# Kernel tuning notes

Hardware: AMD Instinct MI355X
Metric: run time of the kernel (lower is better)

Reference implementation:

```python
import jax, jax.numpy as jnp
import numpy as np

N_HEADS = 16


def setup_inputs() -> dict:
    key = jax.random.key(0)
    ks = jax.random.split(key, 9)
    B, S, D = 2, 2048, 1024
    s = 0.02
    return {
        "x": jax.random.normal(ks[0], (B, S, D), dtype=jnp.float32),
        "Wq": jax.random.normal(ks[1], (D, D), dtype=jnp.float32) * s,
        "bq": jax.random.normal(ks[2], (D,), dtype=jnp.float32) * s,
        "Wk": jax.random.normal(ks[3], (D, D), dtype=jnp.float32) * s,
        "bk": jax.random.normal(ks[4], (D,), dtype=jnp.float32) * s,
        "Wv": jax.random.normal(ks[5], (D, D), dtype=jnp.float32) * s,
        "bv": jax.random.normal(ks[6], (D,), dtype=jnp.float32) * s,
        "Wo": jax.random.normal(ks[7], (D, D), dtype=jnp.float32) * s,
        "bo": jax.random.normal(ks[8], (D,), dtype=jnp.float32) * s,
    }


def reference(x, Wq, bq, Wk, bk, Wv, bv, Wo, bo):
    B, S, D = x.shape
    H = N_HEADS
    hd = D // H
    # projections -> [B, H, S, hd]
    def heads(w, b):
        return (x @ w + b).reshape(B, S, H, hd).transpose(0, 2, 1, 3)
    Q, K, V = heads(Wq, bq), heads(Wk, bk), heads(Wv, bv)
    scores = jnp.einsum("bhqd,bhkd->bhqk", Q, K)
    causal = jnp.triu(jnp.ones((S, S), dtype=bool), k=1)  # True above diagonal
    scores = jnp.where(causal, -jnp.inf, scores)
    w = jax.nn.softmax(scores / jnp.sqrt(jnp.float32(hd)), axis=-1)
    ctx = jnp.einsum("bhqk,bhkd->bhqd", w, V).transpose(0, 2, 1, 3).reshape(B, S, D)
    return ctx @ Wo + bo
```

## Files before the change

### kernel.cpp

```cpp
#include <hip/hip_runtime.h>
#include <hip/hip_bf16.h>

typedef __attribute__((ext_vector_type(8))) short short8;
typedef __attribute__((ext_vector_type(4))) float floatx4;

#define D_MODEL 1024
#define SEQ     2048
#define NB      2
#define NH      16
#define HD      64
#define MROWS   4096
#define CZ      (0.125f * 1.44269504f)

__device__ __forceinline__ floatx4 mfma_bf16(short8 a, short8 b, floatx4 c) {
  return __builtin_amdgcn_mfma_f32_16x16x32_bf16(a, b, c, 0, 0, 0);
}

__device__ __forceinline__ void dma16(const __hip_bfloat16* g, __hip_bfloat16* l) {
  __builtin_amdgcn_global_load_lds(
      (const __attribute__((address_space(1))) void*)g,
      (__attribute__((address_space(3))) void*)l, 16, 0, 0);
}
#define WAIT_VM(n)  __asm__ __volatile__("s_waitcnt vmcnt(" #n ")" ::: "memory")
#define BARRIER()   __asm__ __volatile__("s_barrier" ::: "memory")
#define WAIT_LGKM() __asm__ __volatile__("s_waitcnt lgkmcnt(0)" ::: "memory")

__global__ void convert_x_kernel(const float* __restrict__ x, __hip_bfloat16* __restrict__ xb) {
  int i = (blockIdx.x * 256 + threadIdx.x) * 4;
  float4 v = *(const float4*)(x + i);
  __hip_bfloat16 tmp[4];
  tmp[0] = __float2bfloat16(v.x);
  tmp[1] = __float2bfloat16(v.y);
  tmp[2] = __float2bfloat16(v.z);
  tmp[3] = __float2bfloat16(v.w);
  *(ushort4*)(xb + i) = *(ushort4*)tmp;
}

__global__ void transpose_w_kernel(const float* __restrict__ W0, const float* __restrict__ W1,
                                   const float* __restrict__ W2, const float* __restrict__ W3,
                                   __hip_bfloat16* __restrict__ T0, __hip_bfloat16* __restrict__ T1,
                                   __hip_bfloat16* __restrict__ T2, __hip_bfloat16* __restrict__ T3) {
  const int z = blockIdx.z;
  const float* W = (z == 0) ? W0 : (z == 1) ? W1 : (z == 2) ? W2 : W3;
  __hip_bfloat16* Wt = (z == 0) ? T0 : (z == 1) ? T1 : (z == 2) ? T2 : T3;
  __shared__ float tile[32][33];
  int k0 = blockIdx.x * 32, n0 = blockIdx.y * 32;
  int tx = threadIdx.x, ty = threadIdx.y;
#pragma unroll
  for (int i = 0; i < 4; i++)
    tile[ty + 8 * i][tx] = W[(size_t)(k0 + ty + 8 * i) * D_MODEL + n0 + tx];
  __syncthreads();
#pragma unroll
  for (int i = 0; i < 4; i++)
    Wt[(size_t)(n0 + ty + 8 * i) * D_MODEL + k0 + tx] = __float2bfloat16(tile[tx][ty + 8 * i]);
}

template <int MODE>
__global__ __launch_bounds__(256) void gemm_kernel(
    const __hip_bfloat16* __restrict__ X,
    const __hip_bfloat16* __restrict__ Wt0, const __hip_bfloat16* __restrict__ Wt1,
    const __hip_bfloat16* __restrict__ Wt2,
    const float* __restrict__ b0, const float* __restrict__ b1, const float* __restrict__ b2,
    void* __restrict__ out0, void* __restrict__ out1, void* __restrict__ out2) {
  constexpr int MT = (MODE == 0) ? 128 : 64;
  constexpr int I = MT / 32;
  constexpr int NKT = D_MODEL / 32;

  const int z = blockIdx.y;
  const __hip_bfloat16* Wt = (z == 0) ? Wt0 : (z == 1) ? Wt1 : Wt2;
  const float* bias = (z == 0) ? b0 : (z == 1) ? b1 : b2;
  void* outp = (z == 0) ? out0 : (z == 1) ? out1 : out2;
  const float scale = (MODE == 0 && z == 0) ? CZ : 1.f;

  __shared__ __attribute__((aligned(16))) __hip_bfloat16 As[3][MT * 32];
  __shared__ __attribute__((aligned(16))) __hip_bfloat16 Bs[3][128 * 32];

  const int n0 = blockIdx.x * 128;
  const int m0 = blockIdx.z * MT;
  const int t = threadIdx.x;
  const int lane = t & 63, w = t >> 6;
  const int wm = (w >> 1) * (MT / 2), wn = (w & 1) * 64;
  const int lr = lane & 15;
  const int lq = lane >> 4;

  const __hip_bfloat16* Xp = X + (size_t)m0 * D_MODEL;
  const __hip_bfloat16* Wp = Wt + (size_t)n0 * D_MODEL;

  const int lrow = lane >> 2;
  const int skg = (lane & 3) << 3;
  const int srowA = ((MT == 128) ? (w << 5) : (w << 4)) + lrow;
  const int sbA0 = (((MT == 128) ? (w << 5) : (w << 4)) << 5);
  const int sbA1 = sbA0 + (16 << 5);
  const int srowB = (w << 5) + lrow;
  const int sbB0 = ((w << 5) << 5);
  const int sbB1 = sbB0 + (16 << 5);

#define STAGE_G(kt_, buf_)                                                              \
  {                                                                                     \
    const int kn_ = (kt_) * 32;                                                         \
    dma16(Xp + (size_t)srowA * D_MODEL + kn_ + skg, &As[buf_][sbA0]);                   \
    if (MT == 128) dma16(Xp + (size_t)(srowA + 16) * D_MODEL + kn_ + skg, &As[buf_][sbA1]); \
    dma16(Wp + (size_t)srowB * D_MODEL + kn_ + skg, &Bs[buf_][sbB0]);                   \
    dma16(Wp + (size_t)(srowB + 16) * D_MODEL + kn_ + skg, &Bs[buf_][sbB1]);            \
  }

  floatx4 acc[I][4];
#pragma unroll
  for (int i = 0; i < I; i++)
#pragma unroll
    for (int j = 0; j < 4; j++) acc[i][j] = (floatx4){0.f, 0.f, 0.f, 0.f};

  STAGE_G(0, 0);
  STAGE_G(1, 1);

  int cb = 0;
  for (int kt = 0; kt < NKT; kt++) {
    if (kt < NKT - 1) {
      if constexpr (MODE == 0) WAIT_VM(4);
      else                     WAIT_VM(3);
    } else {
      WAIT_VM(0);
    }
    BARRIER();
    if (kt + 2 < NKT) {
      const int nb = (cb == 0) ? 2 : cb - 1;
      STAGE_G(kt + 2, nb);
    }
    const __hip_bfloat16* Ac = As[cb];
    const __hip_bfloat16* Bc = Bs[cb];
    short8 af[I], bfr[4];
#pragma unroll
    for (int i = 0; i < I; i++) af[i] = *(const short8*)&Ac[(wm + i * 16 + lr) * 32 + lq * 8];
#pragma unroll
    for (int j = 0; j < 4; j++) bfr[j] = *(const short8*)&Bc[(wn + j * 16 + lr) * 32 + lq * 8];
#pragma unroll
    for (int i = 0; i < I; i++)
#pragma unroll
      for (int j = 0; j < 4; j++) acc[i][j] = mfma_bf16(af[i], bfr[j], acc[i][j]);
    cb = (cb == 2) ? 0 : cb + 1;
  }
#undef STAGE_G

#pragma unroll
  for (int j = 0; j < 4; j++) {
    const int n = n0 + wn + j * 16 + lr;
    const float bv = bias[n];
#pragma unroll
    for (int i = 0; i < I; i++) {
      const int mb = m0 + wm + i * 16 + lq * 4;
      if (MODE == 0) {
        __hip_bfloat16* O = (__hip_bfloat16*)outp;
        const int b = mb >> 11, s = mb & 2047;
        const int h = n >> 6, d = n & 63;
        if (z == 2) {
          ushort4 pk;
          __hip_bfloat16* pp = (__hip_bfloat16*)&pk;
#pragma unroll
          for (int r = 0; r < 4; r++) pp[r] = __float2bfloat16(acc[i][j][r] + bv);
          *(ushort4*)(O + (((size_t)(b * NH + h) * HD + d) * SEQ + s)) = pk;
        } else {
#pragma unroll
          for (int r = 0; r < 4; r++)
            O[(((size_t)(b * NH + h) * SEQ + (s + r)) * HD) + d] =
                __float2bfloat16((acc[i][j][r] + bv) * scale);
        }
      } else {
#pragma unroll
        for (int r = 0; r < 4; r++)
          ((float*)outp)[(size_t)(mb + r) * D_MODEL + n] = acc[i][j][r] + bv;
      }
    }
  }
}

__global__ __launch_bounds__(256, 2) void attn_kernel(
    const __hip_bfloat16* __restrict__ Q, const __hip_bfloat16* __restrict__ Kg,
    const __hip_bfloat16* __restrict__ Vt, __hip_bfloat16* __restrict__ ctx) {
  const int bh = blockIdx.x;
  const int b = bh >> 4, h = bh & 15;
  const int p = blockIdx.y;
  const int t = threadIdx.x, lane = t & 63, w = t >> 6;
  const int lr = lane & 15, lq = lane >> 4;

  __shared__ __attribute__((aligned(16))) __hip_bfloat16 Ks[3][64 * 64];
  __shared__ __attribute__((aligned(16))) __hip_bfloat16 VTs[3][64 * 64];
  __shared__ __attribute__((aligned(16))) __hip_bfloat16 Ps[4][16 * 72];

  const __hip_bfloat16* Qb = Q + (size_t)bh * SEQ * HD;
  const __hip_bfloat16* Kb = Kg + (size_t)bh * SEQ * HD;
  const __hip_bfloat16* Vb = Vt + (size_t)bh * HD * SEQ;

  short8 qf[2][2];
#pragma unroll
  for (int ph = 0; ph < 2; ph++) {
    const int qt = ph ? 31 - p : p;
    const int rw = qt * 64 + w * 16;
#pragma unroll
    for (int ks = 0; ks < 2; ks++)
      qf[ph][ks] = *(const short8*)(Qb + (size_t)(rw + lr) * HD + ks * 32 + lq * 8);
  }

  const int srow0 = (w << 4) + (lane >> 3);
  const int sgl = lane & 7;
  const int sb0 = ((w << 4) << 6);
  const int sb1 = (((w << 4) + 8) << 6);

  const int nkt0 = p + 1;
  const int TOT = 33;

#define STAGE(nn, nb)                                                                  \
  {                                                                                    \
    const int r0 = srow0, r1 = srow0 + 8;                                              \
    dma16(Kb + ((size_t)((nn) + r0) << 6) + ((sgl ^ (r0 & 7)) << 3), &Ks[nb][sb0]);    \
    dma16(Kb + ((size_t)((nn) + r1) << 6) + ((sgl ^ (r1 & 7)) << 3), &Ks[nb][sb1]);    \
    dma16(Vb + (size_t)r0 * SEQ + (nn) + ((sgl ^ (r0 & 7)) << 3), &VTs[nb][sb0]);      \
    dma16(Vb + (size_t)r1 * SEQ + (nn) + ((sgl ^ (r1 & 7)) << 3), &VTs[nb][sb1]);      \
  }
#define KTN(gs) (((gs) < nkt0) ? (gs) : (gs)-nkt0)

  STAGE(KTN(0) * 64, 0);
  STAGE(KTN(1) * 64, 1);
  int g = 0, cb = 0;

  for (int ph = 0; ph < 2; ph++) {
    const int qt = ph ? 31 - p : p;
    const int nkt = qt + 1;
    const int rw = qt * 64 + w * 16;

    floatx4 o[4];
#pragma unroll
    for (int dt = 0; dt < 4; dt++) o[dt] = (floatx4){0.f, 0.f, 0.f, 0.f};
    float ls[4] = {0.f, 0.f, 0.f, 0.f};

    for (int kt = 0; kt < nkt; kt++, g++) {
      if (g < TOT - 1) WAIT_VM(4);
      else             WAIT_VM(0);
      BARRIER();
      if (g + 2 < TOT) {
        const int nb = (cb == 0) ? 2 : cb - 1;
        STAGE(KTN(g + 2) * 64, nb);
      }
      const __hip_bfloat16* Kc = Ks[cb];
      const __hip_bfloat16* Vc = VTs[cb];
      cb = (cb == 2) ? 0 : cb + 1;
      __hip_bfloat16* PsW = Ps[w];

      floatx4 s[4];
#pragma unroll
      for (int nt = 0; nt < 4; nt++) s[nt] = (floatx4){0.f, 0.f, 0.f, 0.f};
#pragma unroll
      for (int ks = 0; ks < 2; ks++) {
#pragma unroll
        for (int nt = 0; nt < 4; nt++) {
          const int key = nt * 16 + lr;
          short8 kf = *(const short8*)&Kc[(key << 6) + (((ks * 4 + lq) ^ (key & 7)) << 3)];
          s[nt] = mfma_bf16(qf[ph][ks], kf, s[nt]);
        }
      }

      const int n0 = kt * 64;
      if (kt == nkt - 1) {
#pragma unroll
        for (int nt = 0; nt < 4; nt++)
#pragma unroll
          for (int r = 0; r < 4; r++) {
            const int row = rw + lq * 4 + r;
            const int key = n0 + nt * 16 + lr;
            float pe = (key <= row) ? exp2f(s[nt][r]) : 0.f;
            ls[r] += pe;
            PsW[(lq * 4 + r) * 72 + nt * 16 + lr] = __float2bfloat16(pe);
          }
      } else {
#pragma unroll
        for (int nt = 0; nt < 4; nt++)
#pragma unroll
          for (int r = 0; r < 4; r++) {
            float pe = exp2f(s[nt][r]);
            ls[r] += pe;
            PsW[(lq * 4 + r) * 72 + nt * 16 + lr] = __float2bfloat16(pe);
          }
      }
      WAIT_LGKM();

#pragma unroll
      for (int ks = 0; ks < 2; ks++) {
        short8 pf = *(const short8*)&PsW[lr * 72 + ks * 32 + lq * 8];
#pragma unroll
        for (int dt = 0; dt < 4; dt++) {
          const int d = dt * 16 + lr;
          short8 vf = *(const short8*)&Vc[(d << 6) + (((ks * 4 + lq) ^ (d & 7)) << 3)];
          o[dt] = mfma_bf16(pf, vf, o[dt]);
        }
      }
    }

    float inv[4];
#pragma unroll
    for (int r = 0; r < 4; r++) {
      float v = ls[r];
#pragma unroll
      for (int m = 8; m >= 1; m >>= 1) v += __shfl_xor(v, m, 16);
      inv[r] = 1.f / v;
    }
    __hip_bfloat16* cp = ctx + (size_t)b * SEQ * D_MODEL + h * HD;
#pragma unroll
    for (int dt = 0; dt < 4; dt++)
#pragma unroll
      for (int r = 0; r < 4; r++) {
        const int s = rw + lq * 4 + r;
        cp[(size_t)s * D_MODEL + dt * 16 + lr] = __float2bfloat16(o[dt][r] * inv[r]);
      }
  }
#undef STAGE
#undef KTN
}

extern "C" void kernel_launch(void* const* d_in, const int* in_sizes, int n_in,
                              void* d_out, int out_size, void* d_ws, size_t ws_size,
                              hipStream_t stream) {
  const float* x  = (const float*)d_in[0];
  const float* Wq = (const float*)d_in[1];
  const float* bq = (const float*)d_in[2];
  const float* Wk = (const float*)d_in[3];
  const float* bk = (const float*)d_in[4];
  const float* Wv = (const float*)d_in[5];
  const float* bv = (const float*)d_in[6];
  const float* Wo = (const float*)d_in[7];
  const float* bo = (const float*)d_in[8];

  char* ws = (char*)d_ws;
  const size_t MB = 1u << 20;
  __hip_bfloat16* xb  = (__hip_bfloat16*)(ws + 0 * MB);
  __hip_bfloat16* wtq = (__hip_bfloat16*)(ws + 8 * MB);
  __hip_bfloat16* wtk = (__hip_bfloat16*)(ws + 10 * MB);
  __hip_bfloat16* wtv = (__hip_bfloat16*)(ws + 12 * MB);
  __hip_bfloat16* wto = (__hip_bfloat16*)(ws + 14 * MB);
  __hip_bfloat16* qb  = (__hip_bfloat16*)(ws + 16 * MB);
  __hip_bfloat16* kb  = (__hip_bfloat16*)(ws + 24 * MB);
  __hip_bfloat16* vt  = (__hip_bfloat16*)(ws + 32 * MB);
  __hip_bfloat16* ctx = xb;

  convert_x_kernel<<<4096, 256, 0, stream>>>(x, xb);
  transpose_w_kernel<<<dim3(32, 32, 4), dim3(32, 8), 0, stream>>>(Wq, Wk, Wv, Wo,
                                                                  wtq, wtk, wtv, wto);
  gemm_kernel<0><<<dim3(8, 3, 32), 256, 0, stream>>>(xb, wtq, wtk, wtv, bq, bk, bv,
                                                     (void*)qb, (void*)kb, (void*)vt);
  attn_kernel<<<dim3(32, 16), 256, 0, stream>>>(qb, kb, vt, ctx);
  gemm_kernel<1><<<dim3(8, 1, 64), 256, 0, stream>>>(ctx, wto, wto, wto, bo, bo, bo,
                                                     d_out, d_out, d_out);
}
```

Baseline: 198.4 us.

## Split attention key tiles across two wave groups and keep P in registers

The attention block grows to 512 threads. Each pair of wave groups handles the two 64-key halves of a 128-key tile, and their partial outputs and row sums are merged through LDS at the end. The score MFMA is transposed so the exponentiated P can be reshuffled into operand layout with ds_bpermute instead of a round trip through shared memory. The triple-buffered 64-key staging becomes double-buffered 128-key staging with a full vmcnt wait every iteration. This adds memory-level parallelism but risks less load/compute overlap and idle diagonal waves.

```diff
diff --git a/kernel.cpp b/kernel.cpp
--- a/kernel.cpp
+++ b/kernel.cpp
@@ -3,6 +3,7 @@
 
 typedef __attribute__((ext_vector_type(8))) short short8;
 typedef __attribute__((ext_vector_type(4))) float floatx4;
+typedef __attribute__((ext_vector_type(4))) int intx4;
 
 #define D_MODEL 1024
 #define SEQ     2048
@@ -23,7 +24,12 @@
 }
 #define WAIT_VM(n)  __asm__ __volatile__("s_waitcnt vmcnt(" #n ")" ::: "memory")
 #define BARRIER()   __asm__ __volatile__("s_barrier" ::: "memory")
-#define WAIT_LGKM() __asm__ __volatile__("s_waitcnt lgkmcnt(0)" ::: "memory")
+
+__device__ __forceinline__ int packbf(float a, float b) {
+  union { __hip_bfloat16 h; unsigned short u; } x, y;
+  x.h = __float2bfloat16(a); y.h = __float2bfloat16(b);
+  return (int)(((unsigned)y.u << 16) | (unsigned)x.u);
+}
 
 __global__ void convert_x_kernel(const float* __restrict__ x, __hip_bfloat16* __restrict__ xb) {
   int i = (blockIdx.x * 256 + threadIdx.x) * 4;
@@ -173,7 +179,7 @@
   }
 }
 
-__global__ __launch_bounds__(256, 2) void attn_kernel(
+__global__ __launch_bounds__(512, 4) void attn_kernel(
     const __hip_bfloat16* __restrict__ Q, const __hip_bfloat16* __restrict__ Kg,
     const __hip_bfloat16* __restrict__ Vt, __hip_bfloat16* __restrict__ ctx) {
   const int bh = blockIdx.x;
@@ -181,10 +187,10 @@
   const int p = blockIdx.y;
   const int t = threadIdx.x, lane = t & 63, w = t >> 6;
   const int lr = lane & 15, lq = lane >> 4;
-
-  __shared__ __attribute__((aligned(16))) __hip_bfloat16 Ks[3][64 * 64];
-  __shared__ __attribute__((aligned(16))) __hip_bfloat16 VTs[3][64 * 64];
-  __shared__ __attribute__((aligned(16))) __hip_bfloat16 Ps[4][16 * 72];
+  const int wr = w & 3, wb = w >> 2;
+
+  __shared__ __attribute__((aligned(16))) __hip_bfloat16 Ks[2][128 * 64];
+  __shared__ __attribute__((aligned(16))) __hip_bfloat16 VTs[2][64 * 128];
 
   const __hip_bfloat16* Qb = Q + (size_t)bh * SEQ * HD;
   const __hip_bfloat16* Kb = Kg + (size_t)bh * SEQ * HD;
@@ -194,125 +200,168 @@
 #pragma unroll
   for (int ph = 0; ph < 2; ph++) {
     const int qt = ph ? 31 - p : p;
-    const int rw = qt * 64 + w * 16;
+    const int rw = qt * 64 + wr * 16;
 #pragma unroll
     for (int ks = 0; ks < 2; ks++)
       qf[ph][ks] = *(const short8*)(Qb + (size_t)(rw + lr) * HD + ks * 32 + lq * 8);
   }
 
-  const int srow0 = (w << 4) + (lane >> 3);
-  const int sgl = lane & 7;
-  const int sb0 = ((w << 4) << 6);
-  const int sb1 = (((w << 4) + 8) << 6);
-
-  const int nkt0 = p + 1;
-  const int TOT = 33;
-
-#define STAGE(nn, nb)                                                                  \
-  {                                                                                    \
-    const int r0 = srow0, r1 = srow0 + 8;                                              \
-    dma16(Kb + ((size_t)((nn) + r0) << 6) + ((sgl ^ (r0 & 7)) << 3), &Ks[nb][sb0]);    \
-    dma16(Kb + ((size_t)((nn) + r1) << 6) + ((sgl ^ (r1 & 7)) << 3), &Ks[nb][sb1]);    \
-    dma16(Vb + (size_t)r0 * SEQ + (nn) + ((sgl ^ (r0 & 7)) << 3), &VTs[nb][sb0]);      \
-    dma16(Vb + (size_t)r1 * SEQ + (nn) + ((sgl ^ (r1 & 7)) << 3), &VTs[nb][sb1]);      \
-  }
-#define KTN(gs) (((gs) < nkt0) ? (gs) : (gs)-nkt0)
-
-  STAGE(KTN(0) * 64, 0);
-  STAGE(KTN(1) * 64, 1);
-  int g = 0, cb = 0;
+  const int kr0 = (w << 4) + (lane >> 3);
+  const int kg0 = (lane & 7) ^ (kr0 & 7);
+  const int kr1 = kr0 + 8;
+  const int kg1 = (lane & 7) ^ (kr1 & 7);
+  const int kb0 = (w << 4) << 6;
+  const int kb1 = ((w << 4) + 8) << 6;
+  const int vr0 = (w << 3) + (lane >> 4);
+  const int vg0 = (lane & 15) ^ (vr0 & 15);
+  const int vr1 = vr0 + 4;
+  const int vg1 = (lane & 15) ^ (vr1 & 15);
+  const int vb0 = (w << 3) << 7;
+  const int vb1 = ((w << 3) + 4) << 7;
+
+  const int nktA = (p + 2) >> 1;
+  const int TOT = 17;
+
+#define STAGE(nn, nb)                                                           \
+  {                                                                             \
+    dma16(Kb + ((size_t)((nn) + kr0) << 6) + (kg0 << 3), &Ks[nb][kb0]);         \
+    dma16(Kb + ((size_t)((nn) + kr1) << 6) + (kg1 << 3), &Ks[nb][kb1]);         \
+    dma16(Vb + (size_t)vr0 * SEQ + (nn) + (vg0 << 3), &VTs[nb][vb0]);           \
+    dma16(Vb + (size_t)vr1 * SEQ + (nn) + (vg1 << 3), &VTs[nb][vb1]);           \
+  }
+
+  STAGE(0, 0);
+  int g = 0;
+
+  const int idx0 = (lr + ((lq & 1) << 5)) << 2;
+  const int idx1 = idx0 + 64;
+  const bool hi = (lq >= 2);
 
   for (int ph = 0; ph < 2; ph++) {
     const int qt = ph ? 31 - p : p;
-    const int nkt = qt + 1;
-    const int rw = qt * 64 + w * 16;
+    const int nkt = (qt + 2) >> 1;
+    const int rw = qt * 64 + wr * 16;
+    const int q = rw + lr;
 
     floatx4 o[4];
 #pragma unroll
     for (int dt = 0; dt < 4; dt++) o[dt] = (floatx4){0.f, 0.f, 0.f, 0.f};
-    float ls[4] = {0.f, 0.f, 0.f, 0.f};
+    float ls = 0.f;
 
     for (int kt = 0; kt < nkt; kt++, g++) {
-      if (g < TOT - 1) WAIT_VM(4);
-      else             WAIT_VM(0);
+      WAIT_VM(0);
       BARRIER();
-      if (g + 2 < TOT) {
-        const int nb = (cb == 0) ? 2 : cb - 1;
-        STAGE(KTN(g + 2) * 64, nb);
+      if (g + 1 < TOT) {
+        const int gn = g + 1;
+        const int ktn = (gn < nktA) ? gn : gn - nktA;
+        STAGE(ktn << 7, gn & 1);
       }
-      const __hip_bfloat16* Kc = Ks[cb];
-      const __hip_bfloat16* Vc = VTs[cb];
-      cb = (cb == 2) ? 0 : cb + 1;
-      __hip_bfloat16* PsW = Ps[w];
-
-      floatx4 s[4];
-#pragma unroll
-      for (int nt = 0; nt < 4; nt++) s[nt] = (floatx4){0.f, 0.f, 0.f, 0.f};
-#pragma unroll
-      for (int ks = 0; ks < 2; ks++) {
-#pragma unroll
-        for (int nt = 0; nt < 4; nt++) {
-          const int key = nt * 16 + lr;
-          short8 kf = *(const short8*)&Kc[(key << 6) + (((ks * 4 + lq) ^ (key & 7)) << 3)];
-          s[nt] = mfma_bf16(qf[ph][ks], kf, s[nt]);
+      const int n0 = (kt << 7) + (wb << 6);
+      if (n0 <= rw + 15) {
+        const __hip_bfloat16* Kc = Ks[g & 1];
+        const __hip_bfloat16* Vc = VTs[g & 1];
+
+        floatx4 s[4];
+#pragma unroll
+        for (int nt = 0; nt < 4; nt++) s[nt] = (floatx4){0.f, 0.f, 0.f, 0.f};
+#pragma unroll
+        for (int ks = 0; ks < 2; ks++) {
+#pragma unroll
+          for (int nt = 0; nt < 4; nt++) {
+            const int row = (wb << 6) + (nt << 4) + lr;
+            short8 kf = *(const short8*)&Kc[(row << 6) + ((((ks << 2) + lq) ^ (row & 7)) << 3)];
+            s[nt] = mfma_bf16(kf, qf[ph][ks], s[nt]);
+          }
         }
-      }
-
-      const int n0 = kt * 64;
-      if (kt == nkt - 1) {
-#pragma unroll
-        for (int nt = 0; nt < 4; nt++)
-#pragma unroll
-          for (int r = 0; r < 4; r++) {
-            const int row = rw + lq * 4 + r;
-            const int key = n0 + nt * 16 + lr;
-            float pe = (key <= row) ? exp2f(s[nt][r]) : 0.f;
-            ls[r] += pe;
-            PsW[(lq * 4 + r) * 72 + nt * 16 + lr] = __float2bfloat16(pe);
+
+        int pkA[4], pkB[4];
+        if (n0 + 63 > rw) {
+#pragma unroll
+          for (int nt = 0; nt < 4; nt++) {
+            const int kbase = n0 + (nt << 4) + (lq << 2);
+            float pe[4];
+#pragma unroll
+            for (int r = 0; r < 4; r++) {
+              pe[r] = (kbase + r <= q) ? exp2f(s[nt][r]) : 0.f;
+              ls += pe[r];
+            }
+            pkA[nt] = packbf(pe[0], pe[1]);
+            pkB[nt] = packbf(pe[2], pe[3]);
           }
-      } else {
-#pragma unroll
-        for (int nt = 0; nt < 4; nt++)
-#pragma unroll
-          for (int r = 0; r < 4; r++) {
-            float pe = exp2f(s[nt][r]);
-            ls[r] += pe;
-            PsW[(lq * 4 + r) * 72 + nt * 16 + lr] = __float2bfloat16(pe);
+        } else {
+#pragma unroll
+          for (int nt = 0; nt < 4; nt++) {
+            float pe[4];
+#pragma unroll
+            for (int r = 0; r < 4; r++) {
+              pe[r] = exp2f(s[nt][r]);
+              ls += pe[r];
+            }
+            pkA[nt] = packbf(pe[0], pe[1]);
+            pkB[nt] = packbf(pe[2], pe[3]);
           }
-      }
-      WAIT_LGKM();
-
-#pragma unroll
-      for (int ks = 0; ks < 2; ks++) {
-        short8 pf = *(const short8*)&PsW[lr * 72 + ks * 32 + lq * 8];
-#pragma unroll
-        for (int dt = 0; dt < 4; dt++) {
-          const int d = dt * 16 + lr;
-          short8 vf = *(const short8*)&Vc[(d << 6) + (((ks * 4 + lq) ^ (d & 7)) << 3)];
-          o[dt] = mfma_bf16(pf, vf, o[dt]);
+        }
+
+#pragma unroll
+        for (int ks = 0; ks < 2; ks++) {
+          const int t0 = 2 * ks, t1 = 2 * ks + 1;
+          int c0a = __builtin_amdgcn_ds_bpermute(idx0, pkA[t0]);
+          int c0b = __builtin_amdgcn_ds_bpermute(idx0, pkA[t1]);
+          int c1a = __builtin_amdgcn_ds_bpermute(idx0, pkB[t0]);
+          int c1b = __builtin_amdgcn_ds_bpermute(idx0, pkB[t1]);
+          int c2a = __builtin_amdgcn_ds_bpermute(idx1, pkA[t0]);
+          int c2b = __builtin_amdgcn_ds_bpermute(idx1, pkA[t1]);
+          int c3a = __builtin_amdgcn_ds_bpermute(idx1, pkB[t0]);
+          int c3b = __builtin_amdgcn_ds_bpermute(idx1, pkB[t1]);
+          intx4 bi;
+          bi[0] = hi ? c0b : c0a;
+          bi[1] = hi ? c1b : c1a;
+          bi[2] = hi ? c2b : c2a;
+          bi[3] = hi ? c3b : c3a;
+          short8 pf = __builtin_bit_cast(short8, bi);
+#pragma unroll
+          for (int dt = 0; dt < 4; dt++) {
+            const int row = (dt << 4) + lr;
+            const int gv = (wb << 3) + (ks << 2) + lq;
+            short8 vf = *(const short8*)&Vc[(row << 7) + ((gv ^ (row & 15)) << 3)];
+            o[dt] = mfma_bf16(vf, pf, o[dt]);
+          }
         }
       }
     }
 
-    float inv[4];
-#pragma unroll
-    for (int r = 0; r < 4; r++) {
-      float v = ls[r];
-#pragma unroll
-      for (int m = 8; m >= 1; m >>= 1) v += __shfl_xor(v, m, 16);
-      inv[r] = 1.f / v;
+    const int fb = (g - 1) & 1;
+    BARRIER();
+    {
+      float* od = (float*)&Ks[fb][0];
+      float* ld = (float*)&VTs[fb][0];
+      const int base = (wr << 10) + (lane << 4);
+      if (wb == 1) {
+#pragma unroll
+        for (int dt = 0; dt < 4; dt++) *(floatx4*)&od[base + (dt << 2)] = o[dt];
+        ld[(wr << 6) + lane] = ls;
+      }
+      BARRIER();
+      if (wb == 0) {
+#pragma unroll
+        for (int dt = 0; dt < 4; dt++) o[dt] += *(const floatx4*)&od[base + (dt << 2)];
+        ls += ld[(wr << 6) + lane];
+        ls += __shfl_xor(ls, 16);
+        ls += __shfl_xor(ls, 32);
+        const float inv = 1.f / ls;
+        __hip_bfloat16* cp = ctx + (size_t)b * SEQ * D_MODEL + h * HD + (size_t)q * D_MODEL;
+#pragma unroll
+        for (int dt = 0; dt < 4; dt++) {
+          ushort4 pk;
+          __hip_bfloat16* pp = (__hip_bfloat16*)&pk;
+#pragma unroll
+          for (int r = 0; r < 4; r++) pp[r] = __float2bfloat16(o[dt][r] * inv);
+          *(ushort4*)(cp + (dt << 4) + (lq << 2)) = pk;
+        }
+      }
     }
-    __hip_bfloat16* cp = ctx + (size_t)b * SEQ * D_MODEL + h * HD;
-#pragma unroll
-    for (int dt = 0; dt < 4; dt++)
-#pragma unroll
-      for (int r = 0; r < 4; r++) {
-        const int s = rw + lq * 4 + r;
-        cp[(size_t)s * D_MODEL + dt * 16 + lr] = __float2bfloat16(o[dt][r] * inv[r]);
-      }
   }
 #undef STAGE
-#undef KTN
 }
 
 extern "C" void kernel_launch(void* const* d_in, const int* in_sizes, int n_in,
@@ -345,7 +394,7 @@
                                                                   wtq, wtk, wtv, wto);
   gemm_kernel<0><<<dim3(8, 3, 32), 256, 0, stream>>>(xb, wtq, wtk, wtv, bq, bk, bv,
                                                      (void*)qb, (void*)kb, (void*)vt);
-  attn_kernel<<<dim3(32, 16), 256, 0, stream>>>(qb, kb, vt, ctx);
+  attn_kernel<<<dim3(32, 16), 512, 0, stream>>>(qb, kb, vt, ctx);
   gemm_kernel<1><<<dim3(8, 1, 64), 256, 0, stream>>>(ctx, wto, wto, wto, bo, bo, bo,
                                                      d_out, d_out, d_out);
 }
```

Result: no change. 199.8 us (+0.7%).
